# Optimization experiments

Hardware: AMD Instinct MI355X
Metric: run time of the kernel (lower is better)

The kernel has to match this reference:

```python
import jax, jax.numpy as jnp
import numpy as np

NUM_CODE = 1024
CODE_DIM = 256


def setup_inputs() -> dict:
    key = jax.random.key(0)
    k1, k2 = jax.random.split(key)
    z_e = jax.random.normal(k1, (32, CODE_DIM, 32, 32), dtype=jnp.float32)
    span = 1.0 / NUM_CODE
    codebook = jax.random.uniform(k2, (NUM_CODE, CODE_DIM), dtype=jnp.float32,
                                  minval=-span, maxval=span)
    return {"z_e": z_e, "codebook": codebook}


def reference(z_e, codebook):
    # NCHW -> NHWC
    z = jnp.transpose(z_e, (0, 2, 3, 1))  # [B,H,W,D]
    B, H, W, D = z.shape
    zf = z.reshape(-1, D)  # [N,D]
    cb = jax.lax.stop_gradient(codebook)
    # squared L2 distances via sum-sq + matmul
    d = (jnp.sum(zf * zf, axis=1, keepdims=True)
         + jnp.sum(cb * cb, axis=1)
         - 2.0 * jnp.einsum('nd,kd->nk', zf, cb))  # [N,K]
    indices = jnp.argmin(d, axis=1)  # [N]
    z_q = cb[indices].reshape(B, H, W, D)
    # straight-through estimator
    z_q = z + jax.lax.stop_gradient(z_q - z)
    indices = indices.reshape(B, H, W)
    z_q = jnp.transpose(z_q, (0, 3, 1, 2))  # back to NCHW
    return z_q, indices
```

## Files before the change

### kernel.cpp

```cpp
#include <hip/hip_runtime.h>

#define D_   256
#define HW_  1024
#define N_   32768
#define K_   1024

#define QMARGS 0.12288f

typedef _Float16 half8 __attribute__((ext_vector_type(8)));
typedef __attribute__((ext_vector_type(4))) float f32x4;

#define GLDS(g, l) __builtin_amdgcn_global_load_lds( \
    (const __attribute__((address_space(1))) unsigned int*)(g), \
    (__attribute__((address_space(3))) unsigned int*)(l), 16, 0, 0)


__device__ __forceinline__ float np_sumsq_256(const float* a, int stride) {
    float blk[2];
    #pragma unroll
    for (int h = 0; h < 2; ++h) {
        const float* p = a + (size_t)h * 128 * stride;
        float r[8];
        #pragma unroll
        for (int j = 0; j < 8; ++j) {
            float v = p[(size_t)j * stride];
            r[j] = __fmul_rn(v, v);
        }
        for (int i = 1; i < 16; ++i) {
            #pragma unroll
            for (int j = 0; j < 8; ++j) {
                float v = p[(size_t)(i * 8 + j) * stride];
                r[j] = __fadd_rn(r[j], __fmul_rn(v, v));
            }
        }
        blk[h] = __fadd_rn(__fadd_rn(__fadd_rn(r[0], r[1]), __fadd_rn(r[2], r[3])),
                           __fadd_rn(__fadd_rn(r[4], r[5]), __fadd_rn(r[6], r[7])));
    }
    return __fadd_rn(blk[0], blk[1]);
}

__global__ __launch_bounds__(256) void prep_kernel(const float* __restrict__ z,
                                                   const float* __restrict__ cb,
                                                   float* __restrict__ A32,
                                                   float* __restrict__ B32,
                                                   float* __restrict__ hbF,
                                                   half8* __restrict__ cbAf,
                                                   half8* __restrict__ zBf) {
    const int blk = blockIdx.x;
    const int tid = threadIdx.x;
    if (blk < 4) {
        int k = blk * 256 + tid;
        float v = np_sumsq_256(cb + (size_t)k * D_, 1);
        B32[k] = v;
        hbF[k] = 512.0f * v;
    } else if (blk < 132) {
        int n  = (blk - 4) * 256 + tid;
        int b  = n >> 10;
        int hw = n & 1023;
        A32[n] = np_sumsq_256(z + (size_t)b * (D_ * HW_) + hw, HW_);
    } else if (blk < 260) {
        int c  = (blk - 132) * 256 + tid;
        int kf = c >> 9;
        int ds = (c >> 6) & 7;
        int q  = (c >> 4) & 3;
        int r  = c & 15;
        int k  = kf * 16 + r;
        int d0 = ds * 32 + q * 8;
        const float* src = cb + (size_t)k * D_ + d0;
        half8 v;
        #pragma unroll
        for (int j = 0; j < 8; ++j) v[j] = (_Float16)(src[j] * -1024.0f);
        cbAf[c] = v;
    } else {
        int c    = (blk - 260) * 256 + tid;
        int pxg  = c >> 9;
        int ds   = (c >> 6) & 7;
        int lane = c & 63;
        int q    = lane >> 4;
        int r    = lane & 15;
        int px   = pxg * 16 + r;
        int bb   = px >> 10;
        int hw   = px & 1023;
        int d0   = ds * 32 + q * 8;
        const float* src = z + (size_t)bb * (D_ * HW_) + hw;
        half8 v;
        #pragma unroll
        for (int j = 0; j < 8; ++j) v[j] = (_Float16)src[(size_t)(d0 + j) * HW_];
        zBf[c] = v;
    }
}

#define CSWAP(va, ka, vb, kb) { \
    bool sw = (vb < va) || (vb == va && kb < ka); \
    float tv = va; int tk = ka; \
    va = sw ? vb : va; ka = sw ? kb : ka; \
    vb = sw ? tv : vb; kb = sw ? tk : kb; }

#define TOP4_INS(S, KK, V0,K0,V1,K1,V2,K2,V3,K3) \
    if (S < V3) { \
        if (S < V1) { \
            V3 = V2; K3 = K2; V2 = V1; K2 = K1; \
            if (S < V0) { V1 = V0; K1 = K0; V0 = S; K0 = KK; } \
            else        { V1 = S;  K1 = KK; } \
        } else { \
            if (S < V2) { V3 = V2; K3 = K2; V2 = S; K2 = KK; } \
            else        { V3 = S;  K3 = KK; } \
        } \
    }

#define QMERGE(V0,K0,V1,K1,V2,K2,V3,K3) \
    _Pragma("unroll") \
    for (int off = 16; off <= 32; off <<= 1) { \
        float b0 = __shfl_xor(V0, off, 64), b1 = __shfl_xor(V1, off, 64); \
        float b2 = __shfl_xor(V2, off, 64), b3 = __shfl_xor(V3, off, 64); \
        int   c0 = __shfl_xor(K0, off, 64), c1 = __shfl_xor(K1, off, 64); \
        int   c2 = __shfl_xor(K2, off, 64), c3 = __shfl_xor(K3, off, 64); \
        CSWAP(V0, K0, b3, c3); CSWAP(V1, K1, b2, c2); \
        CSWAP(V2, K2, b1, c1); CSWAP(V3, K3, b0, c0); \
        CSWAP(V0, K0, V2, K2); CSWAP(V1, K1, V3, K3); \
        CSWAP(V0, K0, V1, K1); CSWAP(V2, K2, V3, K3); \
    }

__global__ __launch_bounds__(256, 2) void vq_screen11(
        const half8* __restrict__ zBf,
        const half8* __restrict__ cbAf,
        const float* __restrict__ hbF,
        const float* __restrict__ A32,
        const float* __restrict__ B32,
        const float* __restrict__ cb,
        const float* __restrict__ z,
        float* __restrict__ oidx)
{
    __shared__ half8 abuf[2][2][1024];
    __shared__ float mrg[64 * 8];
    __shared__ int   fcount;
    __shared__ int   fn[64];
    __shared__ int   fck[64][4];

    const int tid  = threadIdx.x;
    const int lane = tid & 63;
    const int wave = tid >> 6;
    const int pxg  = wave >> 1;
    const int kh   = wave & 1;
    const int q    = lane >> 4;
    const int r    = lane & 15;

    if (tid == 0) fcount = 0;

    const int f0 = blockIdx.x * 4 + pxg * 2;
    half8 b0[8], b1[8];
    #pragma unroll
    for (int ds = 0; ds < 8; ++ds) {
        b0[ds] = zBf[(size_t)(f0 * 8 + ds) * 64 + lane];
        b1[ds] = zBf[(size_t)((f0 + 1) * 8 + ds) * 64 + lane];
    }

    const char* gbase = (const char*)cbAf + (size_t)(kh * 16) * 16384
                      + pxg * 8192 + lane * 16;
    const int   ldsOff = pxg * 512;

    {
        char* d = (char*)&abuf[kh][0][ldsOff];
        #pragma unroll
        for (int i = 0; i < 8; ++i) GLDS(gbase + i * 1024, d + i * 1024);
    }
    __syncthreads();

    float v0a = 3.4e38f, v1a = 3.4e38f, v2a = 3.4e38f, v3a = 3.4e38f;
    int   k0a = 0x7fffffff, k1a = 0x7fffffff, k2a = 0x7fffffff, k3a = 0x7fffffff;
    float v0b = 3.4e38f, v1b = 3.4e38f, v2b = 3.4e38f, v3b = 3.4e38f;
    int   k0b = 0x7fffffff, k1b = 0x7fffffff, k2b = 0x7fffffff, k3b = 0x7fffffff;

    for (int chl = 0; chl < 16; ++chl) {
        const int cur = chl & 1;
        if (chl < 15) {
            const char* s = gbase + (size_t)(chl + 1) * 16384;
            char* d = (char*)&abuf[kh][cur ^ 1][ldsOff];
            #pragma unroll
            for (int i = 0; i < 8; ++i) GLDS(s + i * 1024, d + i * 1024);
        }

        const int ch = kh * 16 + chl;
        const float4 h0 = *reinterpret_cast<const float4*>(&hbF[ch * 32 + q * 4]);
        const float4 h1 = *reinterpret_cast<const float4*>(&hbF[ch * 32 + 16 + q * 4]);
        f32x4 a00 = {h0.x, h0.y, h0.z, h0.w};
        f32x4 a01 = a00;
        f32x4 a10 = {h1.x, h1.y, h1.z, h1.w};
        f32x4 a11 = a10;

        #pragma unroll
        for (int ds = 0; ds < 8; ++ds) {
            half8 A0 = abuf[kh][cur][(0 * 8 + ds) * 64 + lane];
            half8 A1 = abuf[kh][cur][(8 + ds) * 64 + lane];
            a00 = __builtin_amdgcn_mfma_f32_16x16x32_f16(A0, b0[ds], a00, 0,0,0);
            a01 = __builtin_amdgcn_mfma_f32_16x16x32_f16(A0, b1[ds], a01, 0,0,0);
            a10 = __builtin_amdgcn_mfma_f32_16x16x32_f16(A1, b0[ds], a10, 0,0,0);
            a11 = __builtin_amdgcn_mfma_f32_16x16x32_f16(A1, b1[ds], a11, 0,0,0);
        }

        float ma = fminf(fminf(fminf(a00[0], a00[1]), fminf(a00[2], a00[3])),
                         fminf(fminf(a10[0], a10[1]), fminf(a10[2], a10[3])));
        float mb = fminf(fminf(fminf(a01[0], a01[1]), fminf(a01[2], a01[3])),
                         fminf(fminf(a11[0], a11[1]), fminf(a11[2], a11[3])));
        if (ma < v3a) {
            #pragma unroll
            for (int i = 0; i < 8; ++i) {
                int kk  = ch * 32 + (i >> 2) * 16 + q * 4 + (i & 3);
                float s = (i < 4) ? a00[i & 3] : a10[i & 3];
                TOP4_INS(s, kk, v0a,k0a, v1a,k1a, v2a,k2a, v3a,k3a);
            }
        }
        if (mb < v3b) {
            #pragma unroll
            for (int i = 0; i < 8; ++i) {
                int kk  = ch * 32 + (i >> 2) * 16 + q * 4 + (i & 3);
                float s = (i < 4) ? a01[i & 3] : a11[i & 3];
                TOP4_INS(s, kk, v0b,k0b, v1b,k1b, v2b,k2b, v3b,k3b);
            }
        }
        __syncthreads();
    }

    QMERGE(v0a,k0a, v1a,k1a, v2a,k2a, v3a,k3a);
    QMERGE(v0b,k0b, v1b,k1b, v2b,k2b, v3b,k3b);

    int* mrgI = (int*)mrg;
    if (kh == 1 && q == 0) {
        int pl0 = pxg * 32 + r;
        mrg[pl0 * 8 + 0] = v0a; mrg[pl0 * 8 + 1] = v1a;
        mrg[pl0 * 8 + 2] = v2a; mrg[pl0 * 8 + 3] = v3a;
        mrgI[pl0 * 8 + 4] = k0a; mrgI[pl0 * 8 + 5] = k1a;
        mrgI[pl0 * 8 + 6] = k2a; mrgI[pl0 * 8 + 7] = k3a;
        int pl1 = pxg * 32 + 16 + r;
        mrg[pl1 * 8 + 0] = v0b; mrg[pl1 * 8 + 1] = v1b;
        mrg[pl1 * 8 + 2] = v2b; mrg[pl1 * 8 + 3] = v3b;
        mrgI[pl1 * 8 + 4] = k0b; mrgI[pl1 * 8 + 5] = k1b;
        mrgI[pl1 * 8 + 6] = k2b; mrgI[pl1 * 8 + 7] = k3b;
    }
    __syncthreads();
    if (kh == 0 && q == 0) {
        #pragma unroll
        for (int set = 0; set < 2; ++set) {
            int pl = pxg * 32 + set * 16 + r;
            float V0 = set ? v0b : v0a, V1 = set ? v1b : v1a;
            float V2 = set ? v2b : v2a, V3 = set ? v3b : v3a;
            int   K0 = set ? k0b : k0a, K1 = set ? k1b : k1a;
            int   K2 = set ? k2b : k2a, K3 = set ? k3b : k3a;
            float o0 = mrg[pl * 8 + 0], o1 = mrg[pl * 8 + 1];
            float o2 = mrg[pl * 8 + 2], o3 = mrg[pl * 8 + 3];
            int   p0 = mrgI[pl * 8 + 4], p1 = mrgI[pl * 8 + 5];
            int   p2 = mrgI[pl * 8 + 6], p3 = mrgI[pl * 8 + 7];
            CSWAP(V0, K0, o3, p3); CSWAP(V1, K1, o2, p2);
            CSWAP(V2, K2, o1, p1); CSWAP(V3, K3, o0, p0);
            CSWAP(V0, K0, V2, K2); CSWAP(V1, K1, V3, K3);
            CSWAP(V0, K0, V1, K1); CSWAP(V2, K2, V3, K3);

            int n = blockIdx.x * 64 + pl;
            oidx[n] = (float)K0;
            if (V1 - V0 < QMARGS) {
                int slot = atomicAdd(&fcount, 1);
                fn[slot] = n;
                fck[slot][0] = K0; fck[slot][1] = K1;
                fck[slot][2] = K2; fck[slot][3] = K3;
            }
        }
    }
    __syncthreads();

    const int fc = fcount;
    for (int i = wave; i < fc; i += 4) {
        const int n  = fn[i];
        const int bb = n >> 10, hw = n & 1023;
        const float* zb = z + (size_t)bb * (D_ * HW_) + hw;
        float zf[4];
        #pragma unroll
        for (int j = 0; j < 4; ++j) zf[j] = zb[(size_t)(lane * 4 + j) * HW_];

        const float An = A32[n];
        float bd = 3.4e38f;
        int   bk = 0x7fffffff;
        #pragma unroll
        for (int c = 0; c < 4; ++c) {
            int k = fck[i][c];
            float4 c4 = *reinterpret_cast<const float4*>(cb + (size_t)k * D_ + lane * 4);
            double acc = 0.0;
            acc = fma((double)c4.x, (double)zf[0], acc);
            acc = fma((double)c4.y, (double)zf[1], acc);
            acc = fma((double)c4.z, (double)zf[2], acc);
            acc = fma((double)c4.w, (double)zf[3], acc);
            #pragma unroll
            for (int off = 1; off <= 32; off <<= 1) acc += __shfl_xor(acc, off, 64);
            float C32 = (float)acc;
            float d32 = __fsub_rn(__fadd_rn(An, B32[k]), __fadd_rn(C32, C32));
            if (d32 < bd || (d32 == bd && k < bk)) { bd = d32; bk = k; }
        }
        if (lane == 0) oidx[n] = (float)bk;
    }
}

__global__ __launch_bounds__(256) void gather_kernel(const float* __restrict__ cb,
                                                     const float* __restrict__ oidx,
                                                     float* __restrict__ zq) {
    const int tid  = threadIdx.x;
    const int s_nl = tid & 63;
    const int s_dw = tid >> 6;
    const int p0   = blockIdx.x * 64;
    const int b    = p0 >> 10;
    const int hw0  = p0 & 1023;

    int idxn = (int)oidx[p0 + s_nl];
    const float4* crow = reinterpret_cast<const float4*>(cb + (size_t)idxn * D_);
    float* zqb = zq + (size_t)b * (D_ * HW_) + hw0;
    #pragma unroll
    for (int r = 0; r < 16; ++r) {
        int d4 = s_dw * 16 + r;
        float4 c4 = crow[d4];
        int d = d4 * 4;
        zqb[(size_t)(d + 0) * HW_ + s_nl] = c4.x;
        zqb[(size_t)(d + 1) * HW_ + s_nl] = c4.y;
        zqb[(size_t)(d + 2) * HW_ + s_nl] = c4.z;
        zqb[(size_t)(d + 3) * HW_ + s_nl] = c4.w;
    }
}

extern "C" void kernel_launch(void* const* d_in, const int* in_sizes, int n_in,
                              void* d_out, int out_size, void* d_ws, size_t ws_size,
                              hipStream_t stream) {
    const float* z  = (const float*)d_in[0];
    const float* cb = (const float*)d_in[1];

    float* zq   = (float*)d_out;
    float* oidx = zq + (size_t)N_ * D_;

    char* ws = (char*)d_ws;
    float* B32  = (float*)(ws + 0);
    float* hbF  = (float*)(ws + 4096);
    float* A32  = (float*)(ws + 8192);
    half8* cbAf = (half8*)(ws + 139264);

    half8* zBf = (half8*)zq;

    prep_kernel<<<4356, 256, 0, stream>>>(z, cb, A32, B32, hbF, cbAf, zBf);
    vq_screen11<<<N_ / 64, 256, 0, stream>>>(
        zBf, cbAf, hbF, A32, B32, cb, z, oidx);
    gather_kernel<<<N_ / 64, 256, 0, stream>>>(cb, oidx, zq);
}
```

Baseline: 93.85 us.

## Split codebook into quarters across blocks and merge top-4 in separate resolve kernel

```diff
diff --git a/kernel.cpp b/kernel.cpp
--- a/kernel.cpp
+++ b/kernel.cpp
@@ -121,162 +121,185 @@
         CSWAP(V0, K0, V1, K1); CSWAP(V2, K2, V3, K3); \
     }
 
-__global__ __launch_bounds__(256, 2) void vq_screen11(
+#define MERGE2(V0,K0,V1,K1,V2,K2,V3,K3, W0,P0,W1,P1,W2,P2,W3,P3) { \
+    CSWAP(V0, K0, W3, P3); CSWAP(V1, K1, W2, P2); \
+    CSWAP(V2, K2, W1, P1); CSWAP(V3, K3, W0, P0); \
+    CSWAP(V0, K0, V2, K2); CSWAP(V1, K1, V3, K3); \
+    CSWAP(V0, K0, V1, K1); CSWAP(V2, K2, V3, K3); }
+
+__global__ __launch_bounds__(256, 4) void vq_screen12(
         const half8* __restrict__ zBf,
         const half8* __restrict__ cbAf,
         const float* __restrict__ hbF,
+        float* __restrict__ st4)
+{
+    __shared__ half8 abuf[2][1024];
+
+    const int tid  = threadIdx.x;
+    const int lane = tid & 63;
+    const int wave = tid >> 6;
+    const int q    = lane >> 4;
+    const int r    = lane & 15;
+
+    const int tile = blockIdx.x >> 2;
+    const int kq   = blockIdx.x & 3;
+
+    const int f0 = tile * 8 + wave * 2;
+    half8 b0[8], b1[8];
+    #pragma unroll
+    for (int ds = 0; ds < 8; ++ds) {
+        b0[ds] = zBf[(size_t)(f0 * 8 + ds) * 64 + lane];
+        b1[ds] = zBf[(size_t)((f0 + 1) * 8 + ds) * 64 + lane];
+    }
+
+    const char* gbase = (const char*)cbAf + (size_t)kq * 131072
+                      + wave * 4096 + lane * 16;
+    const int   ldsOff = wave * 256;
+
+    {
+        char* d = (char*)&abuf[0][ldsOff];
+        #pragma unroll
+        for (int i = 0; i < 4; ++i) GLDS(gbase + i * 1024, d + i * 1024);
+    }
+    __syncthreads();
+
+    float v0a = 3.4e38f, v1a = 3.4e38f, v2a = 3.4e38f, v3a = 3.4e38f;
+    int   k0a = 0x7fffffff, k1a = 0x7fffffff, k2a = 0x7fffffff, k3a = 0x7fffffff;
+    float v0b = 3.4e38f, v1b = 3.4e38f, v2b = 3.4e38f, v3b = 3.4e38f;
+    int   k0b = 0x7fffffff, k1b = 0x7fffffff, k2b = 0x7fffffff, k3b = 0x7fffffff;
+
+    for (int chl = 0; chl < 8; ++chl) {
+        const int cur = chl & 1;
+        if (chl < 7) {
+            const char* s = gbase + (size_t)(chl + 1) * 16384;
+            char* d = (char*)&abuf[cur ^ 1][ldsOff];
+            #pragma unroll
+            for (int i = 0; i < 4; ++i) GLDS(s + i * 1024, d + i * 1024);
+        }
+
+        const int ch = kq * 8 + chl;
+        const float4 h0 = *reinterpret_cast<const float4*>(&hbF[ch * 32 + q * 4]);
+        const float4 h1 = *reinterpret_cast<const float4*>(&hbF[ch * 32 + 16 + q * 4]);
+        f32x4 a00 = {h0.x, h0.y, h0.z, h0.w};
+        f32x4 a01 = a00;
+        f32x4 a10 = {h1.x, h1.y, h1.z, h1.w};
+        f32x4 a11 = a10;
+
+        #pragma unroll
+        for (int ds = 0; ds < 8; ++ds) {
+            half8 A0 = abuf[cur][(0 * 8 + ds) * 64 + lane];
+            half8 A1 = abuf[cur][(8 + ds) * 64 + lane];
+            a00 = __builtin_amdgcn_mfma_f32_16x16x32_f16(A0, b0[ds], a00, 0,0,0);
+            a01 = __builtin_amdgcn_mfma_f32_16x16x32_f16(A0, b1[ds], a01, 0,0,0);
+            a10 = __builtin_amdgcn_mfma_f32_16x16x32_f16(A1, b0[ds], a10, 0,0,0);
+            a11 = __builtin_amdgcn_mfma_f32_16x16x32_f16(A1, b1[ds], a11, 0,0,0);
+        }
+
+        float ma = fminf(fminf(fminf(a00[0], a00[1]), fminf(a00[2], a00[3])),
+                         fminf(fminf(a10[0], a10[1]), fminf(a10[2], a10[3])));
+        float mb = fminf(fminf(fminf(a01[0], a01[1]), fminf(a01[2], a01[3])),
+                         fminf(fminf(a11[0], a11[1]), fminf(a11[2], a11[3])));
+        if (ma < v3a) {
+            #pragma unroll
+            for (int i = 0; i < 8; ++i) {
+                int kk  = ch * 32 + (i >> 2) * 16 + q * 4 + (i & 3);
+                float s = (i < 4) ? a00[i & 3] : a10[i & 3];
+                TOP4_INS(s, kk, v0a,k0a, v1a,k1a, v2a,k2a, v3a,k3a);
+            }
+        }
+        if (mb < v3b) {
+            #pragma unroll
+            for (int i = 0; i < 8; ++i) {
+                int kk  = ch * 32 + (i >> 2) * 16 + q * 4 + (i & 3);
+                float s = (i < 4) ? a01[i & 3] : a11[i & 3];
+                TOP4_INS(s, kk, v0b,k0b, v1b,k1b, v2b,k2b, v3b,k3b);
+            }
+        }
+        __syncthreads();
+    }
+
+    QMERGE(v0a,k0a, v1a,k1a, v2a,k2a, v3a,k3a);
+    QMERGE(v0b,k0b, v1b,k1b, v2b,k2b, v3b,k3b);
+
+    if (q == 0) {
+        {
+            int n = tile * 128 + wave * 32 + r;
+            float* p = st4 + ((size_t)kq * N_ + n) * 8;
+            *reinterpret_cast<float4*>(p)     = make_float4(v0a, v1a, v2a, v3a);
+            *reinterpret_cast<float4*>(p + 4) = make_float4(
+                __int_as_float(k0a), __int_as_float(k1a),
+                __int_as_float(k2a), __int_as_float(k3a));
+        }
+        {
+            int n = tile * 128 + wave * 32 + 16 + r;
+            float* p = st4 + ((size_t)kq * N_ + n) * 8;
+            *reinterpret_cast<float4*>(p)     = make_float4(v0b, v1b, v2b, v3b);
+            *reinterpret_cast<float4*>(p + 4) = make_float4(
+                __int_as_float(k0b), __int_as_float(k1b),
+                __int_as_float(k2b), __int_as_float(k3b));
+        }
+    }
+}
+
+__global__ __launch_bounds__(256) void merge_resolve(
+        const float* __restrict__ st4,
         const float* __restrict__ A32,
         const float* __restrict__ B32,
         const float* __restrict__ cb,
         const float* __restrict__ z,
         float* __restrict__ oidx)
 {
-    __shared__ half8 abuf[2][2][1024];
-    __shared__ float mrg[64 * 8];
     __shared__ int   fcount;
-    __shared__ int   fn[64];
-    __shared__ int   fck[64][4];
+    __shared__ int   fn[256];
+    __shared__ int   fck[256][4];
 
     const int tid  = threadIdx.x;
     const int lane = tid & 63;
     const int wave = tid >> 6;
-    const int pxg  = wave >> 1;
-    const int kh   = wave & 1;
-    const int q    = lane >> 4;
-    const int r    = lane & 15;
+    const int n    = blockIdx.x * 256 + tid;
 
     if (tid == 0) fcount = 0;
-
-    const int f0 = blockIdx.x * 4 + pxg * 2;
-    half8 b0[8], b1[8];
+    __syncthreads();
+
+    float V0, V1, V2, V3; int K0, K1, K2, K3;
+    {
+        const float* p = st4 + (size_t)n * 8;
+        float4 v = *reinterpret_cast<const float4*>(p);
+        float4 kf = *reinterpret_cast<const float4*>(p + 4);
+        V0 = v.x; V1 = v.y; V2 = v.z; V3 = v.w;
+        K0 = __float_as_int(kf.x); K1 = __float_as_int(kf.y);
+        K2 = __float_as_int(kf.z); K3 = __float_as_int(kf.w);
+    }
     #pragma unroll
-    for (int ds = 0; ds < 8; ++ds) {
-        b0[ds] = zBf[(size_t)(f0 * 8 + ds) * 64 + lane];
-        b1[ds] = zBf[(size_t)((f0 + 1) * 8 + ds) * 64 + lane];
-    }
-
-    const char* gbase = (const char*)cbAf + (size_t)(kh * 16) * 16384
-                      + pxg * 8192 + lane * 16;
-    const int   ldsOff = pxg * 512;
-
-    {
-        char* d = (char*)&abuf[kh][0][ldsOff];
-        #pragma unroll
-        for (int i = 0; i < 8; ++i) GLDS(gbase + i * 1024, d + i * 1024);
-    }
-    __syncthreads();
-
-    float v0a = 3.4e38f, v1a = 3.4e38f, v2a = 3.4e38f, v3a = 3.4e38f;
-    int   k0a = 0x7fffffff, k1a = 0x7fffffff, k2a = 0x7fffffff, k3a = 0x7fffffff;
-    float v0b = 3.4e38f, v1b = 3.4e38f, v2b = 3.4e38f, v3b = 3.4e38f;
-    int   k0b = 0x7fffffff, k1b = 0x7fffffff, k2b = 0x7fffffff, k3b = 0x7fffffff;
-
-    for (int chl = 0; chl < 16; ++chl) {
-        const int cur = chl & 1;
-        if (chl < 15) {
-            const char* s = gbase + (size_t)(chl + 1) * 16384;
-            char* d = (char*)&abuf[kh][cur ^ 1][ldsOff];
-            #pragma unroll
-            for (int i = 0; i < 8; ++i) GLDS(s + i * 1024, d + i * 1024);
-        }
-
-        const int ch = kh * 16 + chl;
-        const float4 h0 = *reinterpret_cast<const float4*>(&hbF[ch * 32 + q * 4]);
-        const float4 h1 = *reinterpret_cast<const float4*>(&hbF[ch * 32 + 16 + q * 4]);
-        f32x4 a00 = {h0.x, h0.y, h0.z, h0.w};
-        f32x4 a01 = a00;
-        f32x4 a10 = {h1.x, h1.y, h1.z, h1.w};
-        f32x4 a11 = a10;
-
-        #pragma unroll
-        for (int ds = 0; ds < 8; ++ds) {
-            half8 A0 = abuf[kh][cur][(0 * 8 + ds) * 64 + lane];
-            half8 A1 = abuf[kh][cur][(8 + ds) * 64 + lane];
-            a00 = __builtin_amdgcn_mfma_f32_16x16x32_f16(A0, b0[ds], a00, 0,0,0);
-            a01 = __builtin_amdgcn_mfma_f32_16x16x32_f16(A0, b1[ds], a01, 0,0,0);
-            a10 = __builtin_amdgcn_mfma_f32_16x16x32_f16(A1, b0[ds], a10, 0,0,0);
-            a11 = __builtin_amdgcn_mfma_f32_16x16x32_f16(A1, b1[ds], a11, 0,0,0);
-        }
-
-        float ma = fminf(fminf(fminf(a00[0], a00[1]), fminf(a00[2], a00[3])),
-                         fminf(fminf(a10[0], a10[1]), fminf(a10[2], a10[3])));
-        float mb = fminf(fminf(fminf(a01[0], a01[1]), fminf(a01[2], a01[3])),
-                         fminf(fminf(a11[0], a11[1]), fminf(a11[2], a11[3])));
-        if (ma < v3a) {
-            #pragma unroll
-            for (int i = 0; i < 8; ++i) {
-                int kk  = ch * 32 + (i >> 2) * 16 + q * 4 + (i & 3);
-                float s = (i < 4) ? a00[i & 3] : a10[i & 3];
-                TOP4_INS(s, kk, v0a,k0a, v1a,k1a, v2a,k2a, v3a,k3a);
-            }
-        }
-        if (mb < v3b) {
-            #pragma unroll
-            for (int i = 0; i < 8; ++i) {
-                int kk  = ch * 32 + (i >> 2) * 16 + q * 4 + (i & 3);
-                float s = (i < 4) ? a01[i & 3] : a11[i & 3];
-                TOP4_INS(s, kk, v0b,k0b, v1b,k1b, v2b,k2b, v3b,k3b);
-            }
-        }
-        __syncthreads();
-    }
-
-    QMERGE(v0a,k0a, v1a,k1a, v2a,k2a, v3a,k3a);
-    QMERGE(v0b,k0b, v1b,k1b, v2b,k2b, v3b,k3b);
-
-    int* mrgI = (int*)mrg;
-    if (kh == 1 && q == 0) {
-        int pl0 = pxg * 32 + r;
-        mrg[pl0 * 8 + 0] = v0a; mrg[pl0 * 8 + 1] = v1a;
-        mrg[pl0 * 8 + 2] = v2a; mrg[pl0 * 8 + 3] = v3a;
-        mrgI[pl0 * 8 + 4] = k0a; mrgI[pl0 * 8 + 5] = k1a;
-        mrgI[pl0 * 8 + 6] = k2a; mrgI[pl0 * 8 + 7] = k3a;
-        int pl1 = pxg * 32 + 16 + r;
-        mrg[pl1 * 8 + 0] = v0b; mrg[pl1 * 8 + 1] = v1b;
-        mrg[pl1 * 8 + 2] = v2b; mrg[pl1 * 8 + 3] = v3b;
-        mrgI[pl1 * 8 + 4] = k0b; mrgI[pl1 * 8 + 5] = k1b;
-        mrgI[pl1 * 8 + 6] = k2b; mrgI[pl1 * 8 + 7] = k3b;
-    }
-    __syncthreads();
-    if (kh == 0 && q == 0) {
-        #pragma unroll
-        for (int set = 0; set < 2; ++set) {
-            int pl = pxg * 32 + set * 16 + r;
-            float V0 = set ? v0b : v0a, V1 = set ? v1b : v1a;
-            float V2 = set ? v2b : v2a, V3 = set ? v3b : v3a;
-            int   K0 = set ? k0b : k0a, K1 = set ? k1b : k1a;
-            int   K2 = set ? k2b : k2a, K3 = set ? k3b : k3a;
-            float o0 = mrg[pl * 8 + 0], o1 = mrg[pl * 8 + 1];
-            float o2 = mrg[pl * 8 + 2], o3 = mrg[pl * 8 + 3];
-            int   p0 = mrgI[pl * 8 + 4], p1 = mrgI[pl * 8 + 5];
-            int   p2 = mrgI[pl * 8 + 6], p3 = mrgI[pl * 8 + 7];
-            CSWAP(V0, K0, o3, p3); CSWAP(V1, K1, o2, p2);
-            CSWAP(V2, K2, o1, p1); CSWAP(V3, K3, o0, p0);
-            CSWAP(V0, K0, V2, K2); CSWAP(V1, K1, V3, K3);
-            CSWAP(V0, K0, V1, K1); CSWAP(V2, K2, V3, K3);
-
-            int n = blockIdx.x * 64 + pl;
-            oidx[n] = (float)K0;
-            if (V1 - V0 < QMARGS) {
-                int slot = atomicAdd(&fcount, 1);
-                fn[slot] = n;
-                fck[slot][0] = K0; fck[slot][1] = K1;
-                fck[slot][2] = K2; fck[slot][3] = K3;
-            }
-        }
+    for (int kq = 1; kq < 4; ++kq) {
+        const float* p = st4 + ((size_t)kq * N_ + n) * 8;
+        float4 v = *reinterpret_cast<const float4*>(p);
+        float4 kf = *reinterpret_cast<const float4*>(p + 4);
+        float W0 = v.x, W1 = v.y, W2 = v.z, W3 = v.w;
+        int   P0 = __float_as_int(kf.x), P1 = __float_as_int(kf.y);
+        int   P2 = __float_as_int(kf.z), P3 = __float_as_int(kf.w);
+        MERGE2(V0,K0, V1,K1, V2,K2, V3,K3, W0,P0, W1,P1, W2,P2, W3,P3);
+    }
+
+    oidx[n] = (float)K0;
+    if (V1 - V0 < QMARGS) {
+        int slot = atomicAdd(&fcount, 1);
+        fn[slot] = n;
+        fck[slot][0] = K0; fck[slot][1] = K1;
+        fck[slot][2] = K2; fck[slot][3] = K3;
     }
     __syncthreads();
 
     const int fc = fcount;
     for (int i = wave; i < fc; i += 4) {
-        const int n  = fn[i];
-        const int bb = n >> 10, hw = n & 1023;
+        const int nn = fn[i];
+        const int bb = nn >> 10, hw = nn & 1023;
         const float* zb = z + (size_t)bb * (D_ * HW_) + hw;
         float zf[4];
         #pragma unroll
         for (int j = 0; j < 4; ++j) zf[j] = zb[(size_t)(lane * 4 + j) * HW_];
 
-        const float An = A32[n];
+        const float An = A32[nn];
         float bd = 3.4e38f;
         int   bk = 0x7fffffff;
         #pragma unroll
@@ -294,7 +317,7 @@
             float d32 = __fsub_rn(__fadd_rn(An, B32[k]), __fadd_rn(C32, C32));
             if (d32 < bd || (d32 == bd && k < bk)) { bd = d32; bk = k; }
         }
-        if (lane == 0) oidx[n] = (float)bk;
+        if (lane == 0) oidx[nn] = (float)bk;
     }
 }
 
@@ -338,10 +361,12 @@
     float* A32  = (float*)(ws + 8192);
     half8* cbAf = (half8*)(ws + 139264);
 
-    half8* zBf = (half8*)zq;
+    char*  zqb = (char*)zq;
+    half8* zBf = (half8*)zqb;
+    float* st4 = (float*)(zqb + 16777216);
 
     prep_kernel<<<4356, 256, 0, stream>>>(z, cb, A32, B32, hbF, cbAf, zBf);
-    vq_screen11<<<N_ / 64, 256, 0, stream>>>(
-        zBf, cbAf, hbF, A32, B32, cb, z, oidx);
+    vq_screen12<<<1024, 256, 0, stream>>>(zBf, cbAf, hbF, st4);
+    merge_resolve<<<N_ / 256, 256, 0, stream>>>(st4, A32, B32, cb, z, oidx);
     gather_kernel<<<N_ / 64, 256, 0, stream>>>(cb, oidx, zq);
 }
```

New measurement: 99.23 us. 5.7% more time.
